# Optimization experiments

Hardware: AMD Instinct MI355X
Metric: run time of the kernel (lower is better)

Reference implementation:

```python
import jax, jax.numpy as jnp
import numpy as np

B, N, F_IN, T = 2, 10000, 32, 16
E = 160000
K = 3
C_CHEB = 64
C_TIME = 64
STRIDE = 1
LN_EPS = 1e-5


def setup_inputs() -> dict:
    key = jax.random.key(0)
    ks = jax.random.split(key, 8)
    x = jax.random.normal(ks[0], (B, N, F_IN, T), dtype=jnp.float32)
    edge_index = jax.random.randint(ks[1], (2, E), 0, N, dtype=jnp.int32)
    cheb_W = jax.random.normal(ks[2], (K, F_IN, C_CHEB), dtype=jnp.float32) / np.float32(np.sqrt(F_IN))
    cheb_b = jnp.zeros((C_CHEB,), jnp.float32)
    time_W = jax.random.normal(ks[3], (C_TIME, C_CHEB, 1, 3), dtype=jnp.float32) / np.float32(np.sqrt(C_CHEB * 3))
    time_b = jnp.zeros((C_TIME,), jnp.float32)
    res_W = jax.random.normal(ks[4], (C_TIME, F_IN, 1, 1), dtype=jnp.float32) / np.float32(np.sqrt(F_IN))
    res_b = jnp.zeros((C_TIME,), jnp.float32)
    ln_g = jnp.ones((C_TIME,), jnp.float32)
    ln_b = jnp.zeros((C_TIME,), jnp.float32)
    return dict(x=x, edge_index=edge_index, cheb_W=cheb_W, cheb_b=cheb_b,
                time_W=time_W, time_b=time_b, res_W=res_W, res_b=res_b,
                ln_g=ln_g, ln_b=ln_b)


def _mstgcn_block(x, edge_index, cheb_W, cheb_b, time_W, time_b, res_W, res_b, ln_g, ln_b):
    row, col = edge_index[0], edge_index[1]
    # PyG ChebConv with normalization='sym', lambda_max=2: L_hat = -D^{-1/2} A D^{-1/2}
    deg = jax.ops.segment_sum(jnp.ones((E,), x.dtype), row, num_segments=N)
    dinv = jnp.where(deg > 0, jax.lax.rsqrt(jnp.where(deg > 0, deg, 1.0)), 0.0)
    w = -(dinv[row] * dinv[col])  # (E,)

    def prop(z):  # z: (B,N,F,T) -> L_hat @ z along node axis, all timesteps batched
        zn = jnp.moveaxis(z, 1, 0)                      # (N,B,F,T)
        msg = zn[row] * w[:, None, None, None]          # (E,B,F,T)
        agg = jax.ops.segment_sum(msg, col, num_segments=N)
        return jnp.moveaxis(agg, 0, 1)                  # (B,N,F,T)

    # Chebyshev recursion: Tx0=x, Tx1=L_hat x, Tx_k = 2 L_hat Tx_{k-1} - Tx_{k-2}
    Tx0 = x
    out = jnp.einsum('bnft,fo->bnot', Tx0, cheb_W[0])
    Tx1 = prop(x)
    out = out + jnp.einsum('bnft,fo->bnot', Tx1, cheb_W[1])
    for k in range(2, K):
        Tx2 = 2.0 * prop(Tx1) - Tx0
        out = out + jnp.einsum('bnft,fo->bnot', Tx2, cheb_W[k])
        Tx0, Tx1 = Tx1, Tx2
    out = out + cheb_b[None, None, :, None]

    spatial_gcn = jax.nn.relu(out)                      # (B,N,C_cheb,T)
    spc = jnp.transpose(spatial_gcn, (0, 2, 1, 3))      # (B,C_cheb,N,T)
    tc = jax.lax.conv_general_dilated(
        spc, time_W, window_strides=(1, STRIDE), padding=((0, 0), (1, 1)),
        dimension_numbers=('NCHW', 'OIHW', 'NCHW')) + time_b[None, :, None, None]

    xc = jnp.transpose(x, (0, 2, 1, 3))                 # (B,F_in,N,T)
    res = jax.lax.conv_general_dilated(
        xc, res_W, window_strides=(1, STRIDE), padding=((0, 0), (0, 0)),
        dimension_numbers=('NCHW', 'OIHW', 'NCHW')) + res_b[None, :, None, None]

    z = jax.nn.relu(res + tc)                           # (B,C_time,N,T_out)
    zp = jnp.transpose(z, (0, 3, 2, 1))                 # (B,T_out,N,C_time)
    mu = jnp.mean(zp, axis=-1, keepdims=True)
    var = jnp.mean((zp - mu) ** 2, axis=-1, keepdims=True)
    ln = (zp - mu) * jax.lax.rsqrt(var + LN_EPS) * ln_g + ln_b
    return jnp.transpose(ln, (0, 2, 3, 1))              # (B,N,C_time,T_out)


def reference(x, edge_index, cheb_W, cheb_b, time_W, time_b, res_W, res_b, ln_g, ln_b):
    return _mstgcn_block(x, edge_index, cheb_W, cheb_b, time_W, time_b, res_W, res_b, ln_g, ln_b)
```

## Files before the change

### kernel.cpp

```cpp
#include <hip/hip_runtime.h>


#define F_IN 32
#define TT   16
#define CCH  64
#define FTN  512
#define WPB  4
#define WSTR 1600

__global__ void k_edge1(const int* __restrict__ row, const int* __restrict__ col,
                        float* __restrict__ deg, int* __restrict__ cnt,
                        int* __restrict__ pos, int E) {
    int i = blockIdx.x * 256 + threadIdx.x;
    if (i < E) {
        atomicAdd(&deg[row[i]], 1.0f);
        pos[i] = atomicAdd(&cnt[col[i]], 1);
    }
}

__global__ void k_scan(const int* __restrict__ cnt, int* __restrict__ rowptr, int n) {
    __shared__ int sdata[1024];
    int tid = threadIdx.x;
    int run = 0;
    for (int base = 0; base < n; base += 1024) {
        int v = (base + tid < n) ? cnt[base + tid] : 0;
        sdata[tid] = v;
        __syncthreads();
        for (int off = 1; off < 1024; off <<= 1) {
            int add = (tid >= off) ? sdata[tid - off] : 0;
            __syncthreads();
            sdata[tid] += add;
            __syncthreads();
        }
        int incl  = sdata[tid];
        int total = sdata[1023];
        if (base + tid < n) rowptr[base + tid] = run + incl - v;
        run += total;
        __syncthreads();
    }
    if (tid == 0) rowptr[n] = run;
}

__global__ void k_fill(const int* __restrict__ row, const int* __restrict__ col,
                       const float* __restrict__ deg, const int* __restrict__ rowptr,
                       const int* __restrict__ pos, int* __restrict__ srcs,
                       float* __restrict__ wsort, int E) {
    int i = blockIdx.x * 256 + threadIdx.x;
    if (i < E) {
        int r = row[i], c = col[i];
        float dr = deg[r], dc = deg[c];
        float w = 0.0f;
        if (dr > 0.0f && dc > 0.0f) w = -(rsqrtf(dr) * rsqrtf(dc));
        int slot = rowptr[c] + pos[i];
        srcs[slot]  = r;
        wsort[slot] = w;
    }
}

__global__ void k_prop(const float* __restrict__ zin, float* __restrict__ zout,
                       const int* __restrict__ rowptr, const int* __restrict__ srcs,
                       const float* __restrict__ wsort, int N) {
    int n   = blockIdx.x;
    int tid = threadIdx.x;
    int beg = rowptr[n], end = rowptr[n + 1];
    const size_t bstride = (size_t)N * FTN;
    const size_t eoff = (size_t)(tid >> 7) * bstride + (size_t)(tid & 127) * 4;

    float4 a = make_float4(0.f, 0.f, 0.f, 0.f);
    int j = beg;
    for (; j + 3 < end; j += 4) {
        int   s0 = srcs[j],  s1 = srcs[j + 1], s2 = srcs[j + 2], s3 = srcs[j + 3];
        float w0 = wsort[j], w1 = wsort[j + 1], w2 = wsort[j + 2], w3 = wsort[j + 3];
        float4 v0 = *reinterpret_cast<const float4*>(zin + (size_t)s0 * FTN + eoff);
        float4 v1 = *reinterpret_cast<const float4*>(zin + (size_t)s1 * FTN + eoff);
        float4 v2 = *reinterpret_cast<const float4*>(zin + (size_t)s2 * FTN + eoff);
        float4 v3 = *reinterpret_cast<const float4*>(zin + (size_t)s3 * FTN + eoff);
        a.x = fmaf(w0, v0.x, fmaf(w1, v1.x, fmaf(w2, v2.x, fmaf(w3, v3.x, a.x))));
        a.y = fmaf(w0, v0.y, fmaf(w1, v1.y, fmaf(w2, v2.y, fmaf(w3, v3.y, a.y))));
        a.z = fmaf(w0, v0.z, fmaf(w1, v1.z, fmaf(w2, v2.z, fmaf(w3, v3.z, a.z))));
        a.w = fmaf(w0, v0.w, fmaf(w1, v1.w, fmaf(w2, v2.w, fmaf(w3, v3.w, a.w))));
    }
    for (; j < end; ++j) {
        int   s0 = srcs[j];
        float w0 = wsort[j];
        float4 v0 = *reinterpret_cast<const float4*>(zin + (size_t)s0 * FTN + eoff);
        a.x = fmaf(w0, v0.x, a.x);
        a.y = fmaf(w0, v0.y, a.y);
        a.z = fmaf(w0, v0.z, a.z);
        a.w = fmaf(w0, v0.w, a.w);
    }
    *reinterpret_cast<float4*>(zout + (size_t)n * FTN + eoff) = a;
}

__global__ void k_prep(const float* __restrict__ cheb_W, const float* __restrict__ time_W,
                       const float* __restrict__ res_W,
                       float4* __restrict__ pW4, float4* __restrict__ pT4) {
    int i = blockIdx.x * 256 + threadIdx.x;
    if (i < F_IN * 64) {
        int f = i >> 6, o = i & 63;
        float w0 = cheb_W[(0 * F_IN + f) * 64 + o];
        float w1 = cheb_W[(1 * F_IN + f) * 64 + o];
        float w2 = cheb_W[(2 * F_IN + f) * 64 + o];
        pW4[i] = make_float4(w0 - w2, w1, 2.0f * w2, res_W[o * F_IN + f]);
    }
    if (i < 64 * 64) {
        int ci = i >> 6, co = i & 63;
        pT4[i] = make_float4(time_W[(co * 64 + ci) * 3 + 0],
                             time_W[(co * 64 + ci) * 3 + 1],
                             time_W[(co * 64 + ci) * 3 + 2], 0.0f);
    }
}

__global__ __launch_bounds__(256) void k_fused(
        const float* __restrict__ x, const float* __restrict__ P1, const float* __restrict__ P2,
        const float4* __restrict__ pW4, const float4* __restrict__ pT4,
        const float* __restrict__ cheb_b, const float* __restrict__ time_b,
        const float* __restrict__ res_b, const float* __restrict__ ln_g,
        const float* __restrict__ ln_b, float* __restrict__ out, int N) {
    __shared__ float smem[WPB * WSTR];
    int lane = threadIdx.x & 63;
    int wib  = threadIdx.x >> 6;
    int co   = lane;
    float chb = cheb_b[co], tb = time_b[co], rb = res_b[co];
    float lng = ln_g[co],   lnb = ln_b[co];
    float*  st = smem + wib * WSTR;
    float4* s4 = reinterpret_cast<float4*>(st);

    int gw = blockIdx.x * WPB + wib;
    int nw = gridDim.x * WPB;
    int nitems = 2 * N;
    const size_t bstride = (size_t)N * FTN;

    for (int item = gw; item < nitems; item += nw) {
        int b = (item >= N) ? 1 : 0;
        int n = item - b * N;
        const float4* x4 = reinterpret_cast<const float4*>(x  + b * bstride + (size_t)n * FTN);
        const float4* a4 = reinterpret_cast<const float4*>(P1 + b * bstride + (size_t)n * FTN);
        const float4* b4 = reinterpret_cast<const float4*>(P2 + b * bstride + (size_t)n * FTN);

        float4 xv0 = x4[lane], xv1 = x4[64 + lane];
        float4 av0 = a4[lane], av1 = a4[64 + lane];
        float4 bv0 = b4[lane], bv1 = b4[64 + lane];
        s4[lane]       = xv0;  s4[64 + lane]  = xv1;
        s4[128 + lane] = av0;  s4[192 + lane] = av1;
        s4[256 + lane] = bv0;  s4[320 + lane] = bv1;

        float acc[16], res[16];
#pragma unroll
        for (int t = 0; t < 16; ++t) { acc[t] = chb; res[t] = rb; }

        for (int f = 0; f < F_IN; ++f) {
            float4 wv = pW4[f * 64 + co];
#pragma unroll
            for (int q = 0; q < 4; ++q) {
                float4 xv = s4[f * 4 + q];
                float4 av = s4[128 + f * 4 + q];
                float4 bv = s4[256 + f * 4 + q];
                acc[q*4+0] = fmaf(wv.x, xv.x, fmaf(wv.y, av.x, fmaf(wv.z, bv.x, acc[q*4+0])));
                acc[q*4+1] = fmaf(wv.x, xv.y, fmaf(wv.y, av.y, fmaf(wv.z, bv.y, acc[q*4+1])));
                acc[q*4+2] = fmaf(wv.x, xv.z, fmaf(wv.y, av.z, fmaf(wv.z, bv.z, acc[q*4+2])));
                acc[q*4+3] = fmaf(wv.x, xv.w, fmaf(wv.y, av.w, fmaf(wv.z, bv.w, acc[q*4+3])));
                res[q*4+0] = fmaf(wv.w, xv.x, res[q*4+0]);
                res[q*4+1] = fmaf(wv.w, xv.y, res[q*4+1]);
                res[q*4+2] = fmaf(wv.w, xv.z, res[q*4+2]);
                res[q*4+3] = fmaf(wv.w, xv.w, res[q*4+3]);
            }
        }

        st[co * 20 + 0] = 0.f; st[co * 20 + 17] = 0.f;
        st[co * 20 + 18] = 0.f; st[co * 20 + 19] = 0.f;
#pragma unroll
        for (int t = 0; t < 16; ++t) st[co * 20 + t + 1] = fmaxf(acc[t], 0.f);

#pragma unroll
        for (int t = 0; t < 16; ++t) acc[t] = res[t] + tb;
        for (int ci = 0; ci < 64; ++ci) {
            float4 tv = pT4[ci * 64 + co];
            const float4* srow = reinterpret_cast<const float4*>(st + ci * 20);
            float4 s0 = srow[0], s1 = srow[1], s2 = srow[2], s3 = srow[3], s4v = srow[4];
            float s[20] = { s0.x,s0.y,s0.z,s0.w, s1.x,s1.y,s1.z,s1.w,
                            s2.x,s2.y,s2.z,s2.w, s3.x,s3.y,s3.z,s3.w,
                            s4v.x,s4v.y,s4v.z,s4v.w };
#pragma unroll
            for (int t = 0; t < 16; ++t)
                acc[t] = fmaf(tv.x, s[t], fmaf(tv.y, s[t + 1], fmaf(tv.z, s[t + 2], acc[t])));
        }

        float z[16];
#pragma unroll
        for (int t = 0; t < 16; ++t) {
            float zz = fmaxf(acc[t], 0.f);
            float p1 = zz, p2 = zz * zz;
#pragma unroll
            for (int off = 32; off >= 1; off >>= 1) {
                p1 += __shfl_xor(p1, off);
                p2 += __shfl_xor(p2, off);
            }
            float mu  = p1 * (1.0f / 64.0f);
            float var = p2 * (1.0f / 64.0f) - mu * mu;
            z[t] = (zz - mu) * rsqrtf(var + 1e-5f) * lng + lnb;
        }
        float4* o4 = reinterpret_cast<float4*>(out + (size_t)item * 1024 + co * 16);
        o4[0] = make_float4(z[0],  z[1],  z[2],  z[3]);
        o4[1] = make_float4(z[4],  z[5],  z[6],  z[7]);
        o4[2] = make_float4(z[8],  z[9],  z[10], z[11]);
        o4[3] = make_float4(z[12], z[13], z[14], z[15]);
    }
}

extern "C" void kernel_launch(void* const* d_in, const int* in_sizes, int n_in,
                              void* d_out, int out_size, void* d_ws, size_t ws_size,
                              hipStream_t stream) {
    const float* x      = (const float*)d_in[0];
    const int*   ei     = (const int*)d_in[1];
    const float* cheb_W = (const float*)d_in[2];
    const float* cheb_b = (const float*)d_in[3];
    const float* time_W = (const float*)d_in[4];
    const float* time_b = (const float*)d_in[5];
    const float* res_W  = (const float*)d_in[6];
    const float* res_b  = (const float*)d_in[7];
    const float* ln_g   = (const float*)d_in[8];
    const float* ln_b   = (const float*)d_in[9];
    float* out = (float*)d_out;

    const int N = in_sizes[0] / (2 * F_IN * TT);
    const int E = in_sizes[1] / 2;
    const int* row = ei;
    const int* col = ei + E;

    char* w = (char*)d_ws;
    size_t off = 0;
    auto carve = [&](size_t bytes) { off = (off + 255) & ~(size_t)255; size_t o = off; off += bytes; return o; };
    float*  deg    = (float*) (w + carve((size_t)N * 4));
    int*    cnt    = (int*)   (w + carve((size_t)N * 4));
    int*    rowptr = (int*)   (w + carve((size_t)(N + 1) * 4));
    int*    pos    = (int*)   (w + carve((size_t)E * 4));
    int*    srcs   = (int*)   (w + carve((size_t)E * 4));
    float*  wsort  = (float*) (w + carve((size_t)E * 4));
    float4* pW4    = (float4*)(w + carve((size_t)F_IN * 64 * 16));
    float4* pT4    = (float4*)(w + carve((size_t)64 * 64 * 16));
    float*  P1     = (float*) (w + carve((size_t)2 * N * FTN * 4));
    float*  P2     = (float*) (w + carve((size_t)2 * N * FTN * 4));
    (void)ws_size; (void)n_in; (void)out_size;

    hipMemsetAsync(deg, 0, (size_t)N * 4, stream);
    hipMemsetAsync(cnt, 0, (size_t)N * 4, stream);

    int eb = (E + 255) / 256;
    k_edge1<<<eb, 256, 0, stream>>>(row, col, deg, cnt, pos, E);
    k_scan<<<1, 1024, 0, stream>>>(cnt, rowptr, N);
    k_fill<<<eb, 256, 0, stream>>>(row, col, deg, rowptr, pos, srcs, wsort, E);
    k_prop<<<N, 256, 0, stream>>>(x,  P1, rowptr, srcs, wsort, N);
    k_prop<<<N, 256, 0, stream>>>(P1, P2, rowptr, srcs, wsort, N);
    k_prep<<<16, 256, 0, stream>>>(cheb_W, time_W, res_W, pW4, pT4);

    int items  = 2 * N;
    int blocks = (items + WPB - 1) / WPB;
    k_fused<<<blocks, 64 * WPB, 0, stream>>>(x, P1, P2, pW4, pT4,
                                             cheb_b, time_b, res_b, ln_g, ln_b, out, N);
}
```

Measured before the change: 584.2 us.

## Remap fused kernel lanes to channel-by-time tiles with register-blocked conv

```diff
diff --git a/kernel.cpp b/kernel.cpp
--- a/kernel.cpp
+++ b/kernel.cpp
@@ -6,7 +6,7 @@
 #define CCH  64
 #define FTN  512
 #define WPB  4
-#define WSTR 1600
+#define WSTR 1536
 
 __global__ void k_edge1(const int* __restrict__ row, const int* __restrict__ col,
                         float* __restrict__ deg, int* __restrict__ cnt,
@@ -94,7 +94,7 @@
 
 __global__ void k_prep(const float* __restrict__ cheb_W, const float* __restrict__ time_W,
                        const float* __restrict__ res_W,
-                       float4* __restrict__ pW4, float4* __restrict__ pT4) {
+                       float4* __restrict__ pW4, float4* __restrict__ pTg) {
     int i = blockIdx.x * 256 + threadIdx.x;
     if (i < F_IN * 64) {
         int f = i >> 6, o = i & 63;
@@ -103,28 +103,60 @@
         float w2 = cheb_W[(2 * F_IN + f) * 64 + o];
         pW4[i] = make_float4(w0 - w2, w1, 2.0f * w2, res_W[o * F_IN + f]);
     }
-    if (i < 64 * 64) {
-        int ci = i >> 6, co = i & 63;
-        pT4[i] = make_float4(time_W[(co * 64 + ci) * 3 + 0],
-                             time_W[(co * 64 + ci) * 3 + 1],
-                             time_W[(co * 64 + ci) * 3 + 2], 0.0f);
-    }
-}
-
-__global__ __launch_bounds__(256) void k_fused(
+    if (i < 64 * 3 * 16) {
+        int ci = i / 48, r = i % 48, dt = r >> 4, c0 = r & 15;
+        pTg[i] = make_float4(time_W[((c0      ) * 64 + ci) * 3 + dt],
+                             time_W[((c0 + 16) * 64 + ci) * 3 + dt],
+                             time_W[((c0 + 32) * 64 + ci) * 3 + dt],
+                             time_W[((c0 + 48) * 64 + ci) * 3 + dt]);
+    }
+}
+
+#define P1K(kk)                                                                              \
+    { float4 wv = pW4[f * 64 + c0 + 16 * kk];                                                \
+      acc[kk*4+0] = fmaf(wv.x, xv.x, fmaf(wv.y, av.x, fmaf(wv.z, bv.x, acc[kk*4+0])));       \
+      acc[kk*4+1] = fmaf(wv.x, xv.y, fmaf(wv.y, av.y, fmaf(wv.z, bv.y, acc[kk*4+1])));       \
+      acc[kk*4+2] = fmaf(wv.x, xv.z, fmaf(wv.y, av.z, fmaf(wv.z, bv.z, acc[kk*4+2])));       \
+      acc[kk*4+3] = fmaf(wv.x, xv.w, fmaf(wv.y, av.w, fmaf(wv.z, bv.w, acc[kk*4+3])));       \
+      res[kk*4+0] = fmaf(wv.w, xv.x, res[kk*4+0]);                                           \
+      res[kk*4+1] = fmaf(wv.w, xv.y, res[kk*4+1]);                                           \
+      res[kk*4+2] = fmaf(wv.w, xv.z, res[kk*4+2]);                                           \
+      res[kk*4+3] = fmaf(wv.w, xv.w, res[kk*4+3]); }
+
+#define P2K(kk, w0c, w1c, w2c)                                                               \
+    acc[kk*4+0] = fmaf(w0c, sm1, fmaf(w1c, s0v, fmaf(w2c, s1v, acc[kk*4+0])));               \
+    acc[kk*4+1] = fmaf(w0c, s0v, fmaf(w1c, s1v, fmaf(w2c, s2v, acc[kk*4+1])));               \
+    acc[kk*4+2] = fmaf(w0c, s1v, fmaf(w1c, s2v, fmaf(w2c, s3v, acc[kk*4+2])));               \
+    acc[kk*4+3] = fmaf(w0c, s2v, fmaf(w1c, s3v, fmaf(w2c, s4v, acc[kk*4+3])));
+
+#define P2COMP(W0, W1, W2, R0, R1, R2)                                                       \
+    { float sm1 = R0.w, s0v = R1.x, s1v = R1.y, s2v = R1.z, s3v = R1.w, s4v = R2.x;          \
+      P2K(0, W0.x, W1.x, W2.x)  P2K(1, W0.y, W1.y, W2.y)                                     \
+      P2K(2, W0.z, W1.z, W2.z)  P2K(3, W0.w, W1.w, W2.w) }
+
+__global__ __launch_bounds__(256, 4) void k_fused(
         const float* __restrict__ x, const float* __restrict__ P1, const float* __restrict__ P2,
-        const float4* __restrict__ pW4, const float4* __restrict__ pT4,
+        const float4* __restrict__ pW4, const float4* __restrict__ pTg,
         const float* __restrict__ cheb_b, const float* __restrict__ time_b,
         const float* __restrict__ res_b, const float* __restrict__ ln_g,
         const float* __restrict__ ln_b, float* __restrict__ out, int N) {
     __shared__ float smem[WPB * WSTR];
     int lane = threadIdx.x & 63;
     int wib  = threadIdx.x >> 6;
-    int co   = lane;
-    float chb = cheb_b[co], tb = time_b[co], rb = res_b[co];
-    float lng = ln_g[co],   lnb = ln_b[co];
+    int c0   = lane & 15;
+    int tg   = lane >> 4;
     float*  st = smem + wib * WSTR;
     float4* s4 = reinterpret_cast<float4*>(st);
+
+    float chb[4], tb[4], rb[4], g[4], bb[4];
+#pragma unroll
+    for (int k = 0; k < 4; ++k) {
+        chb[k] = cheb_b[c0 + 16 * k];
+        tb[k]  = time_b[c0 + 16 * k];
+        rb[k]  = res_b[c0 + 16 * k];
+        g[k]   = ln_g[c0 + 16 * k];
+        bb[k]  = ln_b[c0 + 16 * k];
+    }
 
     int gw = blockIdx.x * WPB + wib;
     int nw = gridDim.x * WPB;
@@ -138,73 +170,100 @@
         const float4* a4 = reinterpret_cast<const float4*>(P1 + b * bstride + (size_t)n * FTN);
         const float4* b4 = reinterpret_cast<const float4*>(P2 + b * bstride + (size_t)n * FTN);
 
-        float4 xv0 = x4[lane], xv1 = x4[64 + lane];
-        float4 av0 = a4[lane], av1 = a4[64 + lane];
-        float4 bv0 = b4[lane], bv1 = b4[64 + lane];
-        s4[lane]       = xv0;  s4[64 + lane]  = xv1;
-        s4[128 + lane] = av0;  s4[192 + lane] = av1;
-        s4[256 + lane] = bv0;  s4[320 + lane] = bv1;
+        s4[lane]       = x4[lane];  s4[64 + lane]  = x4[64 + lane];
+        s4[128 + lane] = a4[lane];  s4[192 + lane] = a4[64 + lane];
+        s4[256 + lane] = b4[lane];  s4[320 + lane] = b4[64 + lane];
 
         float acc[16], res[16];
 #pragma unroll
-        for (int t = 0; t < 16; ++t) { acc[t] = chb; res[t] = rb; }
-
+        for (int k = 0; k < 4; ++k)
+#pragma unroll
+            for (int j = 0; j < 4; ++j) { acc[k*4+j] = chb[k]; res[k*4+j] = rb[k]; }
+
+#pragma unroll 4
         for (int f = 0; f < F_IN; ++f) {
-            float4 wv = pW4[f * 64 + co];
-#pragma unroll
-            for (int q = 0; q < 4; ++q) {
-                float4 xv = s4[f * 4 + q];
-                float4 av = s4[128 + f * 4 + q];
-                float4 bv = s4[256 + f * 4 + q];
-                acc[q*4+0] = fmaf(wv.x, xv.x, fmaf(wv.y, av.x, fmaf(wv.z, bv.x, acc[q*4+0])));
-                acc[q*4+1] = fmaf(wv.x, xv.y, fmaf(wv.y, av.y, fmaf(wv.z, bv.y, acc[q*4+1])));
-                acc[q*4+2] = fmaf(wv.x, xv.z, fmaf(wv.y, av.z, fmaf(wv.z, bv.z, acc[q*4+2])));
-                acc[q*4+3] = fmaf(wv.x, xv.w, fmaf(wv.y, av.w, fmaf(wv.z, bv.w, acc[q*4+3])));
-                res[q*4+0] = fmaf(wv.w, xv.x, res[q*4+0]);
-                res[q*4+1] = fmaf(wv.w, xv.y, res[q*4+1]);
-                res[q*4+2] = fmaf(wv.w, xv.z, res[q*4+2]);
-                res[q*4+3] = fmaf(wv.w, xv.w, res[q*4+3]);
+            float4 xv = s4[f * 4 + tg];
+            float4 av = s4[128 + f * 4 + tg];
+            float4 bv = s4[256 + f * 4 + tg];
+            P1K(0) P1K(1) P1K(2) P1K(3)
+        }
+
+#pragma unroll
+        for (int k = 0; k < 4; ++k) {
+            float4 sv = make_float4(fmaxf(acc[k*4+0], 0.f), fmaxf(acc[k*4+1], 0.f),
+                                    fmaxf(acc[k*4+2], 0.f), fmaxf(acc[k*4+3], 0.f));
+            *reinterpret_cast<float4*>(st + (c0 + 16 * k) * 24 + 4 + 4 * tg) = sv;
+        }
+        if (tg == 0) {
+#pragma unroll
+            for (int k = 0; k < 4; ++k) st[(c0 + 16 * k) * 24 + 3] = 0.f;
+        } else if (tg == 1) {
+#pragma unroll
+            for (int k = 0; k < 4; ++k) st[(c0 + 16 * k) * 24 + 20] = 0.f;
+        }
+
+#pragma unroll
+        for (int k = 0; k < 4; ++k)
+#pragma unroll
+            for (int j = 0; j < 4; ++j) acc[k*4+j] = res[k*4+j] + tb[k];
+
+        float4 wA0, wA1, wA2, rA0, rA1, rA2, wB0, wB1, wB2, rB0, rB1, rB2;
+        {
+            wA0 = pTg[c0]; wA1 = pTg[16 + c0]; wA2 = pTg[32 + c0];
+            const float4* sr = reinterpret_cast<const float4*>(st + 4 * tg);
+            rA0 = sr[0]; rA1 = sr[1]; rA2 = sr[2];
+        }
+        for (int ci = 0; ci < 64; ci += 2) {
+            {
+                int cn = ci + 1;
+                wB0 = pTg[cn * 48 + c0]; wB1 = pTg[cn * 48 + 16 + c0]; wB2 = pTg[cn * 48 + 32 + c0];
+                const float4* sr = reinterpret_cast<const float4*>(st + cn * 24 + 4 * tg);
+                rB0 = sr[0]; rB1 = sr[1]; rB2 = sr[2];
             }
-        }
-
-        st[co * 20 + 0] = 0.f; st[co * 20 + 17] = 0.f;
-        st[co * 20 + 18] = 0.f; st[co * 20 + 19] = 0.f;
-#pragma unroll
-        for (int t = 0; t < 16; ++t) st[co * 20 + t + 1] = fmaxf(acc[t], 0.f);
-
-#pragma unroll
-        for (int t = 0; t < 16; ++t) acc[t] = res[t] + tb;
-        for (int ci = 0; ci < 64; ++ci) {
-            float4 tv = pT4[ci * 64 + co];
-            const float4* srow = reinterpret_cast<const float4*>(st + ci * 20);
-            float4 s0 = srow[0], s1 = srow[1], s2 = srow[2], s3 = srow[3], s4v = srow[4];
-            float s[20] = { s0.x,s0.y,s0.z,s0.w, s1.x,s1.y,s1.z,s1.w,
-                            s2.x,s2.y,s2.z,s2.w, s3.x,s3.y,s3.z,s3.w,
-                            s4v.x,s4v.y,s4v.z,s4v.w };
-#pragma unroll
-            for (int t = 0; t < 16; ++t)
-                acc[t] = fmaf(tv.x, s[t], fmaf(tv.y, s[t + 1], fmaf(tv.z, s[t + 2], acc[t])));
-        }
-
-        float z[16];
-#pragma unroll
-        for (int t = 0; t < 16; ++t) {
-            float zz = fmaxf(acc[t], 0.f);
-            float p1 = zz, p2 = zz * zz;
-#pragma unroll
-            for (int off = 32; off >= 1; off >>= 1) {
-                p1 += __shfl_xor(p1, off);
-                p2 += __shfl_xor(p2, off);
+            P2COMP(wA0, wA1, wA2, rA0, rA1, rA2)
+            if (ci + 2 < 64) {
+                int cn = ci + 2;
+                wA0 = pTg[cn * 48 + c0]; wA1 = pTg[cn * 48 + 16 + c0]; wA2 = pTg[cn * 48 + 32 + c0];
+                const float4* sr = reinterpret_cast<const float4*>(st + cn * 24 + 4 * tg);
+                rA0 = sr[0]; rA1 = sr[1]; rA2 = sr[2];
             }
-            float mu  = p1 * (1.0f / 64.0f);
-            float var = p2 * (1.0f / 64.0f) - mu * mu;
-            z[t] = (zz - mu) * rsqrtf(var + 1e-5f) * lng + lnb;
-        }
-        float4* o4 = reinterpret_cast<float4*>(out + (size_t)item * 1024 + co * 16);
-        o4[0] = make_float4(z[0],  z[1],  z[2],  z[3]);
-        o4[1] = make_float4(z[4],  z[5],  z[6],  z[7]);
-        o4[2] = make_float4(z[8],  z[9],  z[10], z[11]);
-        o4[3] = make_float4(z[12], z[13], z[14], z[15]);
+            P2COMP(wB0, wB1, wB2, rB0, rB1, rB2)
+        }
+
+        float zz[16], s1[4] = {0.f, 0.f, 0.f, 0.f}, s2[4] = {0.f, 0.f, 0.f, 0.f};
+#pragma unroll
+        for (int k = 0; k < 4; ++k)
+#pragma unroll
+            for (int j = 0; j < 4; ++j) {
+                float v = fmaxf(acc[k*4+j], 0.f);
+                zz[k*4+j] = v;
+                s1[j] += v;
+                s2[j] = fmaf(v, v, s2[j]);
+            }
+#pragma unroll
+        for (int off = 1; off <= 8; off <<= 1)
+#pragma unroll
+            for (int j = 0; j < 4; ++j) {
+                s1[j] += __shfl_xor(s1[j], off);
+                s2[j] += __shfl_xor(s2[j], off);
+            }
+        float mu[4], rinv[4];
+#pragma unroll
+        for (int j = 0; j < 4; ++j) {
+            mu[j] = s1[j] * (1.0f / 64.0f);
+            float var = s2[j] * (1.0f / 64.0f) - mu[j] * mu[j];
+            rinv[j] = rsqrtf(var + 1e-5f);
+        }
+        float* ob = out + (size_t)item * 1024;
+#pragma unroll
+        for (int k = 0; k < 4; ++k) {
+            float4 o;
+            o.x = (zz[k*4+0] - mu[0]) * rinv[0] * g[k] + bb[k];
+            o.y = (zz[k*4+1] - mu[1]) * rinv[1] * g[k] + bb[k];
+            o.z = (zz[k*4+2] - mu[2]) * rinv[2] * g[k] + bb[k];
+            o.w = (zz[k*4+3] - mu[3]) * rinv[3] * g[k] + bb[k];
+            *reinterpret_cast<float4*>(ob + (c0 + 16 * k) * 16 + 4 * tg) = o;
+        }
     }
 }
 
@@ -238,7 +297,7 @@
     int*    srcs   = (int*)   (w + carve((size_t)E * 4));
     float*  wsort  = (float*) (w + carve((size_t)E * 4));
     float4* pW4    = (float4*)(w + carve((size_t)F_IN * 64 * 16));
-    float4* pT4    = (float4*)(w + carve((size_t)64 * 64 * 16));
+    float4* pTg    = (float4*)(w + carve((size_t)64 * 3 * 16 * 16));
     float*  P1     = (float*) (w + carve((size_t)2 * N * FTN * 4));
     float*  P2     = (float*) (w + carve((size_t)2 * N * FTN * 4));
     (void)ws_size; (void)n_in; (void)out_size;
@@ -252,10 +311,10 @@
     k_fill<<<eb, 256, 0, stream>>>(row, col, deg, rowptr, pos, srcs, wsort, E);
     k_prop<<<N, 256, 0, stream>>>(x,  P1, rowptr, srcs, wsort, N);
     k_prop<<<N, 256, 0, stream>>>(P1, P2, rowptr, srcs, wsort, N);
-    k_prep<<<16, 256, 0, stream>>>(cheb_W, time_W, res_W, pW4, pT4);
+    k_prep<<<16, 256, 0, stream>>>(cheb_W, time_W, res_W, pW4, pTg);
 
     int items  = 2 * N;
     int blocks = (items + WPB - 1) / WPB;
-    k_fused<<<blocks, 64 * WPB, 0, stream>>>(x, P1, P2, pW4, pT4,
+    k_fused<<<blocks, 64 * WPB, 0, stream>>>(x, P1, P2, pW4, pTg,
                                              cheb_b, time_b, res_b, ln_g, ln_b, out, N);
 }
```

Result: slower. 644.5 us (+10.3%).
